# Optimization experiments

Measured on AMD Instinct MI355X. Metric: run time of the kernel, lower is better.

## Reference

```python
import jax, jax.numpy as jnp
import numpy as np
import math

WINDOW = 512
N_HEAD = 16

def setup_inputs() -> dict:
    key = jax.random.key(0)
    ks = jax.random.split(key, 5)
    B, L, D = 2, 4096, 1024
    s = 0.02
    return {
        "x": jax.random.normal(ks[0], (B, L, D), dtype=jnp.float32),
        "Wq": jax.random.normal(ks[1], (D, D), dtype=jnp.float32) * s,
        "bq": jnp.zeros((D,), jnp.float32),
        "Wk": jax.random.normal(ks[2], (D, D), dtype=jnp.float32) * s,
        "bk": jnp.zeros((D,), jnp.float32),
        "Wv": jax.random.normal(ks[3], (D, D), dtype=jnp.float32) * s,
        "bv": jnp.zeros((D,), jnp.float32),
        "Wo": jax.random.normal(ks[4], (D, D), dtype=jnp.float32) * s,
        "bo": jnp.zeros((D,), jnp.float32),
    }

def reference(x, Wq, bq, Wk, bk, Wv, bv, Wo, bo):
    # Chunked sliding-window MHA (eval mode, dropout inactive).
    B, L, D = x.shape
    W, H = WINDOW, N_HEAD
    dh = D // H
    C = L // W  # number of query chunks
    scale = 1.0 / math.sqrt(dh)

    # Project full sequence once (linear, per-token -> identical math).
    q = x @ Wq.T + bq
    k = x @ Wk.T + bk
    v = x @ Wv.T + bv

    # Pad K/V by one window at the front so every chunk sees 2W keys.
    kp = jnp.pad(k, ((0, 0), (W, 0), (0, 0)))
    vp = jnp.pad(v, ((0, 0), (W, 0), (0, 0)))
    idx = jnp.arange(C)[:, None] * W + jnp.arange(2 * W)[None, :]  # [C, 2W] into padded seq
    kc = kp[:, idx].reshape(B, C, 2 * W, H, dh)
    vc = vp[:, idx].reshape(B, C, 2 * W, H, dh)
    qc = q.reshape(B, C, W, H, dh)

    scores = jnp.einsum('bcqhd,bckhd->bchqk', qc, kc) * scale  # [B,C,H,W,2W]
    valid = (idx >= W)  # padded positions (chunk 0's lookback) are invalid
    scores = jnp.where(valid[None, :, None, None, :], scores, jnp.float32(-1e9))
    attn = jax.nn.softmax(scores, axis=-1)
    out = jnp.einsum('bchqk,bckhd->bcqhd', attn, vc).reshape(B, L, D)
    return out @ Wo.T + bo
```

## Files before the change

kernel.cpp:

```cpp
#include <hip/hip_runtime.h>
#include <hip/hip_bf16.h>

typedef __hip_bfloat16 bf16;
typedef __attribute__((ext_vector_type(8))) short bf16x8;
typedef __attribute__((ext_vector_type(4))) float f32x4;
typedef unsigned int u32;
typedef unsigned short u16;

#define MFMA(a,b,c) __builtin_amdgcn_mfma_f32_16x16x32_bf16((a),(b),(c),0,0,0)

__device__ __forceinline__ u16 f32_to_bf16_rtne(float f) {
  u32 b = __builtin_bit_cast(u32, f);
  b += 0x7FFFu + ((b >> 16) & 1u);
  return (u16)(b >> 16);
}
__device__ __forceinline__ u32 pk2bf(float a, float b) {
  u32 ua = __builtin_bit_cast(u32, a); ua += 0x7FFFu + ((ua >> 16) & 1u);
  u32 ub = __builtin_bit_cast(u32, b); ub += 0x7FFFu + ((ub >> 16) & 1u);
  return __builtin_amdgcn_perm(ub, ua, 0x07060302u);
}
__device__ __forceinline__ u32 pk2bf_rtz(float a, float b) {
  return __builtin_amdgcn_perm(__builtin_bit_cast(u32, b),
                               __builtin_bit_cast(u32, a), 0x07060302u);
}
__device__ __forceinline__ uint4 cvt8(uint4 lo, uint4 hi) {
  const float4 fl = __builtin_bit_cast(float4, lo);
  const float4 fh = __builtin_bit_cast(float4, hi);
  uint4 r;
  r.x = pk2bf(fl.x, fl.y); r.y = pk2bf(fl.z, fl.w);
  r.z = pk2bf(fh.x, fh.y); r.w = pk2bf(fh.z, fh.w);
  return r;
}

__device__ __forceinline__ void barrier_lgkm() {
  asm volatile("s_waitcnt lgkmcnt(0)\n\ts_barrier" ::: "memory");
}

typedef const __attribute__((address_space(1))) void* gas_ptr;
typedef __attribute__((address_space(3))) void* las_ptr;
__device__ __forceinline__ void gload_lds16(const void* g, void* l) {
  __builtin_amdgcn_global_load_lds((gas_ptr)g, (las_ptr)l, 16, 0, 0);
}

static constexpr float SL2E = 0.125f * 1.44269504f;

__global__ __launch_bounds__(256)
void cast_all(const float* __restrict__ wq, const float* __restrict__ wk,
              const float* __restrict__ wv, const float* __restrict__ wo,
              const float* __restrict__ x,
              u16* __restrict__ wqkv, u16* __restrict__ wob,
              u16* __restrict__ xb) {
  const size_t DD8 = (size_t)1024 * 1024 / 8;
  if (blockIdx.x < 2048) {
    const int m = blockIdx.x >> 9;
    const size_t i = ((size_t)(blockIdx.x & 511)) * 256 + threadIdx.x;
    const float* src = (m == 0) ? wq : (m == 1) ? wk : (m == 2) ? wv : wo;
    u16* dst = (m < 3) ? (wqkv + (size_t)m * DD8 * 8) : wob;
    const float4* s = (const float4*)src + i * 2;
    ((uint4*)dst)[i] = cvt8(__builtin_bit_cast(uint4, s[0]),
                            __builtin_bit_cast(uint4, s[1]));
  } else {
    const size_t i = ((size_t)(blockIdx.x - 2048)) * 256 + threadIdx.x;
    const float4* s = (const float4*)x + i * 2;
    ((uint4*)xb)[i] = cvt8(__builtin_bit_cast(uint4, s[0]),
                           __builtin_bit_cast(uint4, s[1]));
  }
}

__global__ __launch_bounds__(512, 2)
void gemm_qkv(const bf16* __restrict__ A, const bf16* __restrict__ W,
              const float* __restrict__ b0, const float* __restrict__ b1,
              const float* __restrict__ b2, u16* __restrict__ o0,
              u16* __restrict__ o1, u16* __restrict__ o2,
              int M, int N, int K)
{
  __shared__ __align__(16) bf16 AsB[2][128 * 64];
  __shared__ __align__(16) bf16 BsB[2][256 * 64];

  const int nwg = gridDim.x * gridDim.y;
  const int raw = blockIdx.y * gridDim.x + blockIdx.x;
  const int vwg = (raw & 7) * (nwg >> 3) + (raw >> 3);
  const int NT  = gridDim.y;
  const int bx  = vwg / NT, by = vwg - bx * NT;
  const int m0  = bx * 128, n0 = by * 256;

  const int tid  = threadIdx.x;
  const int wv   = tid >> 6, lane = tid & 63;
  const int quad = lane >> 4, l16 = lane & 15;
  const int wm   = wv >> 2, wn = wv & 3;
  const int r7   = l16 & 7;

  const int rr = tid >> 3, g = tid & 7;
  const int sg8 = (g ^ (rr & 7)) * 8;
  const bf16* aS = A + (size_t)(m0 + rr) * K + sg8;
  const bf16* wS = W + (size_t)(n0 + rr) * K + sg8;
  const int ldstW = wv * 512;

#define STA8(buf, kt) do { \
    gload_lds16(aS + (size_t)(kt) * 64,                      &AsB[buf][ldstW]); \
    gload_lds16(aS + (size_t)64 * K + (size_t)(kt) * 64,     &AsB[buf][4096 + ldstW]); \
  } while (0)
#define STB8(buf, kt) do { \
    gload_lds16(wS + (size_t)(kt) * 64,                      &BsB[buf][ldstW]); \
    gload_lds16(wS + (size_t)64 * K + (size_t)(kt) * 64,     &BsB[buf][4096 + ldstW]); \
    gload_lds16(wS + (size_t)128 * K + (size_t)(kt) * 64,    &BsB[buf][8192 + ldstW]); \
    gload_lds16(wS + (size_t)192 * K + (size_t)(kt) * 64,    &BsB[buf][12288 + ldstW]); \
  } while (0)

  int aoff[4], boff[4];
#pragma unroll
  for (int mt = 0; mt < 4; ++mt) aoff[mt] = (wm * 64 + mt * 16 + l16) * 64;
#pragma unroll
  for (int nt = 0; nt < 4; ++nt) boff[nt] = (wn * 64 + nt * 16 + l16) * 64;
  const int k0o = (quad ^ r7) * 8;
  const int k1o = ((4 + quad) ^ r7) * 8;

  f32x4 acc[4][4] = {};
  bf16x8 bfr[4][2], afr[2][2];

  const int nk = K >> 6;

  STA8(0, 0);
  STB8(0, 0);
  STB8(1, 1);
  asm volatile("s_waitcnt vmcnt(4)\n\ts_barrier" ::: "memory");

  for (int t = 0; t < nk; ++t) {
    const int c = t & 1;
    const bf16* Ac = AsB[c];
    const bf16* Bc = BsB[c];

#pragma unroll
    for (int nt = 0; nt < 4; ++nt) {
      bfr[nt][0] = *(const bf16x8*)(Bc + boff[nt] + k0o);
      bfr[nt][1] = *(const bf16x8*)(Bc + boff[nt] + k1o);
    }
#pragma unroll
    for (int mt = 0; mt < 2; ++mt) {
      afr[mt][0] = *(const bf16x8*)(Ac + aoff[mt] + k0o);
      afr[mt][1] = *(const bf16x8*)(Ac + aoff[mt] + k1o);
    }
    if (t + 1 < nk) STA8((t + 1) & 1, t + 1);
    asm volatile("s_barrier" ::: "memory");
    __builtin_amdgcn_s_setprio(1);
#pragma unroll
    for (int mt = 0; mt < 2; ++mt)
#pragma unroll
      for (int nt = 0; nt < 4; ++nt) {
        acc[mt][nt] = MFMA(afr[mt][0], bfr[nt][0], acc[mt][nt]);
        acc[mt][nt] = MFMA(afr[mt][1], bfr[nt][1], acc[mt][nt]);
      }
    __builtin_amdgcn_s_setprio(0);
    asm volatile("s_waitcnt lgkmcnt(0)\n\ts_barrier" ::: "memory");

#pragma unroll
    for (int mt = 0; mt < 2; ++mt) {
      afr[mt][0] = *(const bf16x8*)(Ac + aoff[mt + 2] + k0o);
      afr[mt][1] = *(const bf16x8*)(Ac + aoff[mt + 2] + k1o);
    }
    if (t + 2 < nk) STB8(c, t + 2);
    asm volatile("s_barrier" ::: "memory");
    __builtin_amdgcn_s_setprio(1);
#pragma unroll
    for (int mt = 0; mt < 2; ++mt)
#pragma unroll
      for (int nt = 0; nt < 4; ++nt) {
        acc[mt + 2][nt] = MFMA(afr[mt][0], bfr[nt][0], acc[mt + 2][nt]);
        acc[mt + 2][nt] = MFMA(afr[mt][1], bfr[nt][1], acc[mt + 2][nt]);
      }
    __builtin_amdgcn_s_setprio(0);
    if (t + 1 < nk) {
      if (t + 2 < nk)
        asm volatile("s_waitcnt vmcnt(4) lgkmcnt(0)\n\ts_barrier" ::: "memory");
      else
        asm volatile("s_waitcnt vmcnt(0) lgkmcnt(0)\n\ts_barrier" ::: "memory");
    }
  }
#undef STA8
#undef STB8

  const int band = n0 >> 10;
  const float* bias = (band == 0) ? b0 : (band == 1) ? b1 : b2;
#pragma unroll
  for (int nt = 0; nt < 4; ++nt) {
    const int col = n0 + wn * 64 + nt * 16 + l16;
    const int cl  = col & 1023;
    const float bv = bias[cl];
#pragma unroll
    for (int mt = 0; mt < 4; ++mt) {
      const int rbase = m0 + wm * 64 + mt * 16 + quad * 4;
      if (band == 2) {
        const int hh = cl >> 6, dd = cl & 63;
        const int bb = rbase >> 12, tl = rbase & 4095;
        u16* dst = o2 + ((size_t)((bb * 16 + hh) * 64 + dd)) * 4096 + tl;
        uint2 pk;
        pk.x = pk2bf(acc[mt][nt][0] + bv, acc[mt][nt][1] + bv);
        pk.y = pk2bf(acc[mt][nt][2] + bv, acc[mt][nt][3] + bv);
        *(uint2*)dst = pk;
      } else {
        u16* dst = (band == 0) ? o0 : o1;
        const float sc = (band == 0) ? SL2E : 1.0f;
#pragma unroll
        for (int r = 0; r < 4; ++r)
          dst[(size_t)(rbase + r) * 1024 + cl] =
              f32_to_bf16_rtne((acc[mt][nt][r] + bv) * sc);
      }
    }
  }
}

__global__ __launch_bounds__(256)
void gemm_out(const bf16* __restrict__ A, const bf16* __restrict__ W,
              const float* __restrict__ bias, float* __restrict__ out,
              int M, int N, int K)
{
  __shared__ bf16 As[128 * 64];
  __shared__ bf16 Bs[128 * 64];

  const int tid  = threadIdx.x;
  const int wave = tid >> 6, lane = tid & 63;
  const int quad = lane >> 4, l16 = lane & 15;
  const int wm   = wave >> 1, wn  = wave & 1;
  const int m0   = blockIdx.x * 128, n0 = blockIdx.y * 128;

  const int srow = lane >> 3;
  const int sg   = lane & 7;
  const size_t rgs = (size_t)8 * K;
  const bf16* aSrc = A + (size_t)(m0 + wave * 32 + srow) * K + ((sg ^ srow) * 8);
  const bf16* wSrc = W + (size_t)(n0 + wave * 32 + srow) * K + ((sg ^ srow) * 8);
  bf16* aB = As + wave * 32 * 64;
  bf16* wB = Bs + wave * 32 * 64;

  const int niter = K >> 6;

  f32x4 acc[4][4] = {};

  const int arow[4] = { (wm * 64 + 0 * 16 + l16) * 64, (wm * 64 + 1 * 16 + l16) * 64,
                        (wm * 64 + 2 * 16 + l16) * 64, (wm * 64 + 3 * 16 + l16) * 64 };
  const int brow[4] = { (wn * 64 + 0 * 16 + l16) * 64, (wn * 64 + 1 * 16 + l16) * 64,
                        (wn * 64 + 2 * 16 + l16) * 64, (wn * 64 + 3 * 16 + l16) * 64 };
  const int r7 = l16 & 7;

  for (int t = 0; t < niter; ++t) {
    gload_lds16(aSrc,            aB);
    gload_lds16(aSrc + rgs,      aB + 512);
    gload_lds16(aSrc + 2 * rgs,  aB + 1024);
    gload_lds16(aSrc + 3 * rgs,  aB + 1536);
    gload_lds16(wSrc,            wB);
    gload_lds16(wSrc + rgs,      wB + 512);
    gload_lds16(wSrc + 2 * rgs,  wB + 1024);
    gload_lds16(wSrc + 3 * rgs,  wB + 1536);
    aSrc += 64; wSrc += 64;
    __syncthreads();

#pragma unroll
    for (int kk = 0; kk < 2; ++kk) {
      bf16x8 af[4], bw[4];
#pragma unroll
      for (int mt = 0; mt < 4; ++mt)
        af[mt] = *(const bf16x8*)(As + arow[mt] + (((kk * 4 + quad) ^ r7) * 8));
#pragma unroll
      for (int nt = 0; nt < 4; ++nt)
        bw[nt] = *(const bf16x8*)(Bs + brow[nt] + (((kk * 4 + quad) ^ r7) * 8));
#pragma unroll
      for (int mt = 0; mt < 4; ++mt)
#pragma unroll
        for (int nt = 0; nt < 4; ++nt)
          acc[mt][nt] = MFMA(af[mt], bw[nt], acc[mt][nt]);
    }
    if (t + 1 < niter) __syncthreads();
  }

#pragma unroll
  for (int nt = 0; nt < 4; ++nt) {
    const int col = n0 + wn * 64 + nt * 16 + l16;
    const float bv = bias[col & 1023];
#pragma unroll
    for (int mt = 0; mt < 4; ++mt) {
      const int rbase = m0 + wm * 64 + mt * 16 + quad * 4;
#pragma unroll
      for (int r = 0; r < 4; ++r)
        out[(size_t)(rbase + r) * N + col] = acc[mt][nt][r] + bv;
    }
  }
}

__global__ __launch_bounds__(256)
void attn_swin(const bf16* __restrict__ qb, const bf16* __restrict__ kb,
               const bf16* __restrict__ vtb, u16* __restrict__ ctx)
{
  __shared__ __align__(16) bf16 Ks[2][64 * 72];
  __shared__ __align__(16) bf16 Vts[2][64 * 72];

  int bid = blockIdx.x;
  const int g  = bid & 255, qt = bid >> 8;
  const int h  = g & 15, c = (g >> 4) & 7, b = g >> 7;

  const int tid  = threadIdx.x;
  const int w    = tid >> 6, lane = tid & 63;
  const int quad = lane >> 4, l16 = lane & 15;

  const int tq0  = c * 512 + qt * 128;
  const int hoff = h * 64;
  const int kstart = (c == 0) ? 0 : (c - 1) * 512;
  const int nkt    = (c == 0) ? 8 : 16;

  bf16x8 qf[2][2];
#pragma unroll
  for (int u = 0; u < 2; ++u) {
    const bf16* qr = qb + ((size_t)(b * 4096 + tq0 + w * 32 + u * 16 + l16)) * 1024 + hoff;
    qf[u][0] = *(const bf16x8*)(qr + quad * 8);
    qf[u][1] = *(const bf16x8*)(qr + 32 + quad * 8);
  }

  const int m    = tid >> 2;
  const int cseg = (tid & 3) * 16;
  const int sig  = (((m >> 4) & 1) << 5) | (((m >> 2) & 3) << 3)
                 | (((m >> 5) & 1) << 2) | (m & 3);
  const bf16* kgp = kb + ((size_t)(b * 4096 + kstart + sig)) * 1024 + hoff + cseg;
  const bf16* vgp = vtb + ((size_t)((b * 16 + h) * 64 + m)) * 4096 + kstart + cseg;
  const int soff = m * 72 + cseg;

  float l_i[2] = {0.f, 0.f};
  f32x4 o[2][4] = {};

  uint4 ka0 = *(const uint4*)(kgp), ka1 = *(const uint4*)(kgp + 8);
  uint4 va0 = *(const uint4*)(vgp), va1 = *(const uint4*)(vgp + 8);
  kgp += (size_t)64 * 1024; vgp += 64;
  *(uint4*)(Ks[0] + soff) = ka0; *(uint4*)(Ks[0] + soff + 8) = ka1;
  *(uint4*)(Vts[0] + soff) = va0; *(uint4*)(Vts[0] + soff + 8) = va1;
  ka0 = *(const uint4*)(kgp); ka1 = *(const uint4*)(kgp + 8);
  va0 = *(const uint4*)(vgp); va1 = *(const uint4*)(vgp + 8);
  kgp += (size_t)64 * 1024; vgp += 64;
  barrier_lgkm();

  typedef union { u32 d[4]; bf16x8 v; } fragu;

  auto compute = [&](const bf16* ksb, const bf16* vtsb) {
    f32x4 s[2][4] = {};
#pragma unroll
    for (int kt = 0; kt < 4; ++kt) {
      const bf16* kr = ksb + (kt * 16 + l16) * 72;
      bf16x8 kf0 = *(const bf16x8*)(kr + quad * 8);
      bf16x8 kf1 = *(const bf16x8*)(kr + 32 + quad * 8);
      s[0][kt] = MFMA(kf0, qf[0][0], s[0][kt]);
      s[0][kt] = MFMA(kf1, qf[0][1], s[0][kt]);
      s[1][kt] = MFMA(kf0, qf[1][0], s[1][kt]);
      s[1][kt] = MFMA(kf1, qf[1][1], s[1][kt]);
    }
    fragu pf[2][2];
#pragma unroll
    for (int u = 0; u < 2; ++u) {
      float rs = 0.f;
#pragma unroll
      for (int kt = 0; kt < 4; ++kt)
#pragma unroll
        for (int r = 0; r < 4; ++r) {
          const float p = __builtin_amdgcn_exp2f(s[u][kt][r]);
          s[u][kt][r] = p;
          rs += p;
        }
      rs += __shfl_xor(rs, 16);
      rs += __shfl_xor(rs, 32);
      l_i[u] += rs;
#pragma unroll
      for (int hh = 0; hh < 2; ++hh)
#pragma unroll
        for (int dw = 0; dw < 4; ++dw) {
          const int kt = 2 * (dw >> 1) + hh, r0 = 2 * (dw & 1);
          pf[u][hh].d[dw] = pk2bf_rtz(s[u][kt][r0], s[u][kt][r0 + 1]);
        }
    }
#pragma unroll
    for (int dt = 0; dt < 4; ++dt) {
      const bf16* vr = vtsb + (dt * 16 + l16) * 72;
      bf16x8 vf0 = *(const bf16x8*)(vr + quad * 8);
      bf16x8 vf1 = *(const bf16x8*)(vr + 32 + quad * 8);
      o[0][dt] = MFMA(vf0, pf[0][0].v, o[0][dt]);
      o[0][dt] = MFMA(vf1, pf[0][1].v, o[0][dt]);
      o[1][dt] = MFMA(vf0, pf[1][0].v, o[1][dt]);
      o[1][dt] = MFMA(vf1, pf[1][1].v, o[1][dt]);
    }
  };

  for (int t = 0; t < nkt; t += 2) {
    *(uint4*)(Ks[1] + soff) = ka0; *(uint4*)(Ks[1] + soff + 8) = ka1;
    *(uint4*)(Vts[1] + soff) = va0; *(uint4*)(Vts[1] + soff + 8) = va1;
    if (t + 2 < nkt) {
      ka0 = *(const uint4*)(kgp); ka1 = *(const uint4*)(kgp + 8);
      va0 = *(const uint4*)(vgp); va1 = *(const uint4*)(vgp + 8);
      kgp += (size_t)64 * 1024; vgp += 64;
    }
    compute(Ks[0], Vts[0]);
    barrier_lgkm();

    if (t + 2 < nkt) {
      *(uint4*)(Ks[0] + soff) = ka0; *(uint4*)(Ks[0] + soff + 8) = ka1;
      *(uint4*)(Vts[0] + soff) = va0; *(uint4*)(Vts[0] + soff + 8) = va1;
      if (t + 3 < nkt) {
        ka0 = *(const uint4*)(kgp); ka1 = *(const uint4*)(kgp + 8);
        va0 = *(const uint4*)(vgp); va1 = *(const uint4*)(vgp + 8);
        kgp += (size_t)64 * 1024; vgp += 64;
      }
    }
    compute(Ks[1], Vts[1]);
    barrier_lgkm();
  }

#pragma unroll
  for (int u = 0; u < 2; ++u) {
    const float inv = 1.0f / l_i[u];
    const int qrow = tq0 + w * 32 + u * 16 + l16;
    u16* crow = ctx + ((size_t)(b * 4096 + qrow)) * 1024 + hoff;
#pragma unroll
    for (int dt = 0; dt < 4; ++dt) {
      uint2 pk;
      pk.x = pk2bf(o[u][dt][0] * inv, o[u][dt][1] * inv);
      pk.y = pk2bf(o[u][dt][2] * inv, o[u][dt][3] * inv);
      *(uint2*)(crow + dt * 16 + quad * 4) = pk;
    }
  }
}

extern "C" void kernel_launch(void* const* d_in, const int* in_sizes, int n_in,
                              void* d_out, int out_size, void* d_ws, size_t ws_size,
                              hipStream_t stream) {
  const float* x  = (const float*)d_in[0];
  const float* Wq = (const float*)d_in[1];
  const float* bq = (const float*)d_in[2];
  const float* Wk = (const float*)d_in[3];
  const float* bk = (const float*)d_in[4];
  const float* Wv = (const float*)d_in[5];
  const float* bv = (const float*)d_in[6];
  const float* Wo = (const float*)d_in[7];
  const float* bo = (const float*)d_in[8];

  const size_t MD = (size_t)8192 * 1024;
  const size_t DD = (size_t)1024 * 1024;

  char* ws = (char*)d_ws;
  u16*  Wqkvb = (u16*)ws;                     ws += 3 * DD * 2;
  u16*  Wob   = (u16*)ws;                     ws += DD * 2;
  u16*  qbuf  = (u16*)ws;                     ws += MD * 2;
  u16*  kbuf  = (u16*)ws;                     ws += MD * 2;
  u16*  vtb   = (u16*)ws;                     ws += MD * 2;
  u16*  ctx   = (u16*)ws;

  u16* xb = ctx;

  cast_all<<<dim3(6144), dim3(256), 0, stream>>>(Wq, Wk, Wv, Wo, x,
                                                 Wqkvb, Wob, xb);

  gemm_qkv<<<dim3(64, 12), dim3(512), 0, stream>>>(
      (const bf16*)xb, (const bf16*)Wqkvb, bq, bk, bv,
      qbuf, kbuf, vtb, 8192, 3072, 1024);

  attn_swin<<<dim3(1024), dim3(256), 0, stream>>>(
      (const bf16*)qbuf, (const bf16*)kbuf, (const bf16*)vtb, ctx);

  gemm_out<<<dim3(64, 8), dim3(256), 0, stream>>>(
      (const bf16*)ctx, (const bf16*)Wob, bo, (float*)d_out, 8192, 1024, 1024);
}
```

Baseline: 240.2 us.

## Fuse fp32-to-bf16 cast of x into the QKV GEMM A-tile loads

The QKV GEMM now reads the fp32 activations x directly. It converts each A tile to bf16 in registers and writes it to swizzled LDS, replacing the global-to-LDS direct loads of a pre-cast bf16 buffer. The separate cast kernel now converts only the weights, which removes a full read and write pass over x. In exchange the GEMM reads twice as many A bytes, and those bytes are re-read across the N tiles. The A prefetch also now goes through registers, which adds VGPR pressure and conversion ALU work inside the main loop.

```diff
diff --git a/kernel.cpp b/kernel.cpp
--- a/kernel.cpp
+++ b/kernel.cpp
@@ -45,30 +45,21 @@
 static constexpr float SL2E = 0.125f * 1.44269504f;
 
 __global__ __launch_bounds__(256)
-void cast_all(const float* __restrict__ wq, const float* __restrict__ wk,
-              const float* __restrict__ wv, const float* __restrict__ wo,
-              const float* __restrict__ x,
-              u16* __restrict__ wqkv, u16* __restrict__ wob,
-              u16* __restrict__ xb) {
+void cast_w(const float* __restrict__ wq, const float* __restrict__ wk,
+            const float* __restrict__ wv, const float* __restrict__ wo,
+            u16* __restrict__ wqkv, u16* __restrict__ wob) {
   const size_t DD8 = (size_t)1024 * 1024 / 8;
-  if (blockIdx.x < 2048) {
-    const int m = blockIdx.x >> 9;
-    const size_t i = ((size_t)(blockIdx.x & 511)) * 256 + threadIdx.x;
-    const float* src = (m == 0) ? wq : (m == 1) ? wk : (m == 2) ? wv : wo;
-    u16* dst = (m < 3) ? (wqkv + (size_t)m * DD8 * 8) : wob;
-    const float4* s = (const float4*)src + i * 2;
-    ((uint4*)dst)[i] = cvt8(__builtin_bit_cast(uint4, s[0]),
-                            __builtin_bit_cast(uint4, s[1]));
-  } else {
-    const size_t i = ((size_t)(blockIdx.x - 2048)) * 256 + threadIdx.x;
-    const float4* s = (const float4*)x + i * 2;
-    ((uint4*)xb)[i] = cvt8(__builtin_bit_cast(uint4, s[0]),
-                           __builtin_bit_cast(uint4, s[1]));
-  }
+  const int m = blockIdx.x >> 9;
+  const size_t i = ((size_t)(blockIdx.x & 511)) * 256 + threadIdx.x;
+  const float* src = (m == 0) ? wq : (m == 1) ? wk : (m == 2) ? wv : wo;
+  u16* dst = (m < 3) ? (wqkv + (size_t)m * DD8 * 8) : wob;
+  const float4* s = (const float4*)src + i * 2;
+  ((uint4*)dst)[i] = cvt8(__builtin_bit_cast(uint4, s[0]),
+                          __builtin_bit_cast(uint4, s[1]));
 }
 
 __global__ __launch_bounds__(512, 2)
-void gemm_qkv(const bf16* __restrict__ A, const bf16* __restrict__ W,
+void gemm_qkv(const float* __restrict__ A, const bf16* __restrict__ W,
               const float* __restrict__ b0, const float* __restrict__ b1,
               const float* __restrict__ b2, u16* __restrict__ o0,
               u16* __restrict__ o1, u16* __restrict__ o2,
@@ -90,16 +81,11 @@
   const int wm   = wv >> 2, wn = wv & 3;
   const int r7   = l16 & 7;
 
-  const int rr = tid >> 3, g = tid & 7;
-  const int sg8 = (g ^ (rr & 7)) * 8;
-  const bf16* aS = A + (size_t)(m0 + rr) * K + sg8;
-  const bf16* wS = W + (size_t)(n0 + rr) * K + sg8;
+  const int rr8 = tid >> 3, g = tid & 7;
+  const int sg8 = (g ^ (rr8 & 7)) * 8;
+  const bf16* wS = W + (size_t)(n0 + rr8) * K + sg8;
   const int ldstW = wv * 512;
 
-#define STA8(buf, kt) do { \
-    gload_lds16(aS + (size_t)(kt) * 64,                      &AsB[buf][ldstW]); \
-    gload_lds16(aS + (size_t)64 * K + (size_t)(kt) * 64,     &AsB[buf][4096 + ldstW]); \
-  } while (0)
 #define STB8(buf, kt) do { \
     gload_lds16(wS + (size_t)(kt) * 64,                      &BsB[buf][ldstW]); \
     gload_lds16(wS + (size_t)64 * K + (size_t)(kt) * 64,     &BsB[buf][4096 + ldstW]); \
@@ -107,6 +93,11 @@
     gload_lds16(wS + (size_t)192 * K + (size_t)(kt) * 64,    &BsB[buf][12288 + ldstW]); \
   } while (0)
 
+  const int arw = tid >> 2, aj = tid & 3, ae = arw & 7;
+  const float* aF = A + (size_t)(m0 + arw) * K + aj * 16;
+  const int aw0 = arw * 64 + (((2 * aj) ^ ae) * 8);
+  const int aw1 = arw * 64 + ((((2 * aj) + 1) ^ ae) * 8);
+
   int aoff[4], boff[4];
 #pragma unroll
   for (int mt = 0; mt < 4; ++mt) aoff[mt] = (wm * 64 + mt * 16 + l16) * 64;
@@ -117,19 +108,28 @@
 
   f32x4 acc[4][4] = {};
   bf16x8 bfr[4][2], afr[2][2];
+  uint4 pa0, pa1, pa2, pa3;
 
   const int nk = K >> 6;
 
-  STA8(0, 0);
+  pa0 = *(const uint4*)(aF);      pa1 = *(const uint4*)(aF + 4);
+  pa2 = *(const uint4*)(aF + 8);  pa3 = *(const uint4*)(aF + 12);
+  *(uint4*)(AsB[0] + aw0) = cvt8(pa0, pa1);
+  *(uint4*)(AsB[0] + aw1) = cvt8(pa2, pa3);
   STB8(0, 0);
   STB8(1, 1);
-  asm volatile("s_waitcnt vmcnt(4)\n\ts_barrier" ::: "memory");
+  asm volatile("s_waitcnt vmcnt(4) lgkmcnt(0)\n\ts_barrier" ::: "memory");
 
   for (int t = 0; t < nk; ++t) {
     const int c = t & 1;
     const bf16* Ac = AsB[c];
     const bf16* Bc = BsB[c];
 
+    if (t + 1 < nk) {
+      const float* ap = aF + (t + 1) * 64;
+      pa0 = *(const uint4*)(ap);      pa1 = *(const uint4*)(ap + 4);
+      pa2 = *(const uint4*)(ap + 8);  pa3 = *(const uint4*)(ap + 12);
+    }
 #pragma unroll
     for (int nt = 0; nt < 4; ++nt) {
       bfr[nt][0] = *(const bf16x8*)(Bc + boff[nt] + k0o);
@@ -140,7 +140,6 @@
       afr[mt][0] = *(const bf16x8*)(Ac + aoff[mt] + k0o);
       afr[mt][1] = *(const bf16x8*)(Ac + aoff[mt] + k1o);
     }
-    if (t + 1 < nk) STA8((t + 1) & 1, t + 1);
     asm volatile("s_barrier" ::: "memory");
     __builtin_amdgcn_s_setprio(1);
 #pragma unroll
@@ -157,6 +156,11 @@
     for (int mt = 0; mt < 2; ++mt) {
       afr[mt][0] = *(const bf16x8*)(Ac + aoff[mt + 2] + k0o);
       afr[mt][1] = *(const bf16x8*)(Ac + aoff[mt + 2] + k1o);
+    }
+    if (t + 1 < nk) {
+      bf16* Ad = AsB[(t + 1) & 1];
+      *(uint4*)(Ad + aw0) = cvt8(pa0, pa1);
+      *(uint4*)(Ad + aw1) = cvt8(pa2, pa3);
     }
     if (t + 2 < nk) STB8(c, t + 2);
     asm volatile("s_barrier" ::: "memory");
@@ -176,7 +180,6 @@
         asm volatile("s_waitcnt vmcnt(0) lgkmcnt(0)\n\ts_barrier" ::: "memory");
     }
   }
-#undef STA8
 #undef STB8
 
   const int band = n0 >> 10;
@@ -446,13 +449,10 @@
   u16*  vtb   = (u16*)ws;                     ws += MD * 2;
   u16*  ctx   = (u16*)ws;
 
-  u16* xb = ctx;
-
-  cast_all<<<dim3(6144), dim3(256), 0, stream>>>(Wq, Wk, Wv, Wo, x,
-                                                 Wqkvb, Wob, xb);
+  cast_w<<<dim3(2048), dim3(256), 0, stream>>>(Wq, Wk, Wv, Wo, Wqkvb, Wob);
 
   gemm_qkv<<<dim3(64, 12), dim3(512), 0, stream>>>(
-      (const bf16*)xb, (const bf16*)Wqkvb, bq, bk, bv,
+      x, (const bf16*)Wqkvb, bq, bk, bv,
       qbuf, kbuf, vtb, 8192, 3072, 1024);
 
   attn_swin<<<dim3(1024), dim3(256), 0, stream>>>(
```

Result: slower. 279.1 us (+16.2%).
